# Kernel tuning notes

Hardware: AMD Instinct MI355X
Metric: run time of the kernel (lower is better)

## Reference

```python
import jax, jax.numpy as jnp
import numpy as np

TEMPERATURE = 8.0  # sqrt(d_k=64)

def setup_inputs() -> dict:
    key = jax.random.key(0)
    kq, kk, kv, km1, km2 = jax.random.split(key, 5)
    B, Lq, Lk, D = 128, 512, 512, 64
    q = jax.random.normal(kq, (B, Lq, D), dtype=jnp.float32)
    k = jax.random.normal(kk, (B, Lk, D), dtype=jnp.float32)
    v = jax.random.normal(kv, (B, Lk, D), dtype=jnp.float32)
    key_mask = jax.random.bernoulli(km1, 0.5, (B, Lq, Lk))
    query_mask = jax.random.bernoulli(km2, 0.5, (B, Lq, Lk))
    return {"q": q, "k": k, "v": v, "key_mask": key_mask, "query_mask": query_mask}

def reference(q, k, v, key_mask, query_mask):
    # attn = (q @ k^T) / temperature, pre-softmax key masking with -inf
    scores = jnp.einsum('bqd,bkd->bqk', q, k) / TEMPERATURE
    scores = jnp.where(key_mask, -jnp.inf, scores)
    attn = jax.nn.softmax(scores, axis=-1)
    # post-softmax query-row zeroing
    attn = jnp.where(query_mask, 0.0, attn)
    # dropout omitted (eval mode / deterministic reference)
    output = jnp.einsum('bqk,bkd->bqd', attn, v)
    return (output, attn)
```

## Files before the change

### kernel.cpp

```cpp
#include <hip/hip_runtime.h>
#include <hip/hip_bf16.h>

#define BATCH 128
#define LQ    512
#define LK    512
#define DH    64
#define TQ    16
#define KC    128

#define KSTR  72
#define VROW  136
#define SSTR  520

typedef float    float4v __attribute__((ext_vector_type(4)));
typedef short    short8v __attribute__((ext_vector_type(8)));
typedef short    short4v __attribute__((ext_vector_type(4)));
typedef int      int4v   __attribute__((ext_vector_type(4)));
typedef _Float16 half4v  __attribute__((ext_vector_type(4)));

__device__ __forceinline__ short bf16r(float f) {
  union { float f; unsigned u; } x; x.f = f;
  unsigned r = x.u + 0x7FFFu + ((x.u >> 16) & 1u);
  return (short)(r >> 16);
}

__global__ __launch_bounds__(256, 4)
void sdpa_kernel(const float* __restrict__ Q, const float* __restrict__ K,
                 const float* __restrict__ V, const int* __restrict__ KM,
                 const int* __restrict__ QM, float* __restrict__ OUT,
                 float* __restrict__ ATT)
{
  __shared__ short kvs[KC * KSTR];
  __shared__ short scs[TQ * SSTR];

  const int b    = blockIdx.x >> 5;
  const int q0   = (blockIdx.x & 31) * TQ;
  const int tid  = threadIdx.x;
  const int lane = tid & 63;
  const int wave = tid >> 6;
  const int lm   = lane & 15;
  const int quad = lane >> 4;

  const int row = tid >> 4;
  const int col = tid & 15;
  const size_t gro = (size_t)(b * LQ + q0 + row) * LK;

  int4v kmv[8];
#pragma unroll
  for (int j = 0; j < 8; ++j)
    kmv[j] = *(const int4v*)(KM + gro + col * 4 + j * 64);

  const float* qrow = Q + ((size_t)(b * LQ + q0 + lm)) * DH + quad * 8;
  short8v aq0, aq1;
  {
    float4v f0 = *(const float4v*)(qrow + 0);
    float4v f1 = *(const float4v*)(qrow + 4);
    float4v f2 = *(const float4v*)(qrow + 32);
    float4v f3 = *(const float4v*)(qrow + 36);
#pragma unroll
    for (int e = 0; e < 4; ++e) {
      aq0[e]     = bf16r(f0[e]);
      aq0[e + 4] = bf16r(f1[e]);
      aq1[e]     = bf16r(f2[e]);
      aq1[e + 4] = bf16r(f3[e]);
    }
  }

  for (int kt = 0; kt < LK / KC; ++kt) {
    const float* ksrc = K + ((size_t)(b * LK + kt * KC)) * DH;
#pragma unroll
    for (int i = 0; i < 8; ++i) {
      int fl = (tid + i * 256) << 2;
      int r  = fl >> 6, c = fl & 63;
      float4v d4 = *(const float4v*)(ksrc + fl);
      short4v s4;
      s4[0] = bf16r(d4[0]); s4[1] = bf16r(d4[1]);
      s4[2] = bf16r(d4[2]); s4[3] = bf16r(d4[3]);
      *(short4v*)&kvs[r * KSTR + c] = s4;
    }
    __syncthreads();
#pragma unroll
    for (int t = 0; t < 2; ++t) {
      int ntl = (wave * 2 + t) * 16;
      const short* bp = &kvs[(ntl + lm) * KSTR + quad * 8];
      short8v b0 = *(const short8v*)(bp);
      short8v b1 = *(const short8v*)(bp + 32);
      float4v acc = {0.f, 0.f, 0.f, 0.f};
      acc = __builtin_amdgcn_mfma_f32_16x16x32_bf16(aq0, b0, acc, 0, 0, 0);
      acc = __builtin_amdgcn_mfma_f32_16x16x32_bf16(aq1, b1, acc, 0, 0, 0);
      int n  = kt * KC + ntl + lm;
      int m0 = quad * 4;
#pragma unroll
      for (int j = 0; j < 4; ++j)
        *(_Float16*)&scs[(m0 + j) * SSTR + n] = (_Float16)acc[j];
    }
    __syncthreads();
  }

  float s[32];
  float mx = -INFINITY;
#pragma unroll
  for (int j = 0; j < 8; ++j) {
    half4v h4 = *(const half4v*)&scs[row * SSTR + col * 4 + j * 64];
#pragma unroll
    for (int e = 0; e < 4; ++e) {
      float val = kmv[j][e] ? -INFINITY : (float)h4[e];
      s[j * 4 + e] = val;
      mx = fmaxf(mx, val);
    }
  }
  int4v qmv[8];
#pragma unroll
  for (int j = 0; j < 8; ++j)
    qmv[j] = *(const int4v*)(QM + gro + col * 4 + j * 64);
#pragma unroll
  for (int off = 8; off; off >>= 1) mx = fmaxf(mx, __shfl_xor(mx, off, 64));
  float sum = 0.f;
#pragma unroll
  for (int j = 0; j < 32; ++j) {
    float p = __expf((s[j] - mx) * 0.125f);
    s[j] = p;
    sum += p;
  }
#pragma unroll
  for (int off = 8; off; off >>= 1) sum += __shfl_xor(sum, off, 64);
  const float inv = 1.f / sum;
  float* arow = ATT + gro;
#pragma unroll
  for (int j = 0; j < 8; ++j) {
    int kk = col * 4 + j * 64;
    float4v a4;
#pragma unroll
    for (int e = 0; e < 4; ++e)
      a4[e] = qmv[j][e] ? 0.f : s[j * 4 + e] * inv;
    *(float4v*)(arow + kk) = a4;
    short4v ab;
    ab[0] = bf16r(a4[0]); ab[1] = bf16r(a4[1]);
    ab[2] = bf16r(a4[2]); ab[3] = bf16r(a4[3]);
    *(short4v*)&scs[row * SSTR + kk] = ab;
  }

  float4v oacc = {0.f, 0.f, 0.f, 0.f};
  for (int kt = 0; kt < LK / KC; ++kt) {
    const float* vsrc = V + ((size_t)(b * LK + kt * KC)) * DH;
#pragma unroll
    for (int it = 0; it < 2; ++it) {
      int Bx = tid + 256 * it;
      int bR = Bx >> 4;
      int bC = Bx & 15;
      const float* vp = vsrc + bR * 4 * DH + bC * 4;
      float4v r0 = *(const float4v*)(vp);
      float4v r1 = *(const float4v*)(vp + DH);
      float4v r2 = *(const float4v*)(vp + 2 * DH);
      float4v r3 = *(const float4v*)(vp + 3 * DH);
#pragma unroll
      for (int e = 0; e < 4; ++e) {
        int d  = bC * 4 + e;
        int gp = bR ^ (d & 31);
        short4v s4;
        s4[0] = bf16r(r0[e]); s4[1] = bf16r(r1[e]);
        s4[2] = bf16r(r2[e]); s4[3] = bf16r(r3[e]);
        *(short4v*)&kvs[d * VROW + gp * 4] = s4;
      }
    }
    __syncthreads();
#pragma unroll
    for (int ks = 0; ks < 4; ++ks) {
      const short* ap = &scs[lm * SSTR + kt * KC + ks * 32 + quad * 8];
      short8v a8 = *(const short8v*)ap;
      int n  = wave * 16 + lm;
      int g0 = ks * 8 + quad * 2;
      short4v lo = *(const short4v*)&kvs[n * VROW + ((g0    ) ^ (n & 31)) * 4];
      short4v hi = *(const short4v*)&kvs[n * VROW + ((g0 + 1) ^ (n & 31)) * 4];
      short8v b8;
      b8[0] = lo[0]; b8[1] = lo[1]; b8[2] = lo[2]; b8[3] = lo[3];
      b8[4] = hi[0]; b8[5] = hi[1]; b8[6] = hi[2]; b8[7] = hi[3];
      oacc = __builtin_amdgcn_mfma_f32_16x16x32_bf16(a8, b8, oacc, 0, 0, 0);
    }
    __syncthreads();
  }
  {
    int m0 = quad * 4;
    float* obase = OUT + ((size_t)(b * LQ + q0 + m0)) * DH + wave * 16 + lm;
    obase[0 * DH] = oacc[0];
    obase[1 * DH] = oacc[1];
    obase[2 * DH] = oacc[2];
    obase[3 * DH] = oacc[3];
  }
}

extern "C" void kernel_launch(void* const* d_in, const int* in_sizes, int n_in,
                              void* d_out, int out_size, void* d_ws, size_t ws_size,
                              hipStream_t stream) {
  const float* q  = (const float*)d_in[0];
  const float* k  = (const float*)d_in[1];
  const float* v  = (const float*)d_in[2];
  const int*   km = (const int*)d_in[3];
  const int*   qm = (const int*)d_in[4];
  float* out  = (float*)d_out;
  float* attn = out + (size_t)BATCH * LQ * DH;
  dim3 grid(BATCH * (LQ / TQ));
  dim3 block(256);
  hipLaunchKernelGGL(sdpa_kernel, grid, block, 0, stream,
                     q, k, v, km, qm, out, attn);
}
```

Measured before the change: 378.9 us.

## Load K directly to registers, double-buffer V tiles, remap blocks, use nontemporal I/O

The QK^T phase now has each wave load its own K rows from global memory straight into MFMA operands, which removes the LDS staging and two barriers per tile. The PV phase uses 64-key tiles with register prefetch of the next V tile, overlapping the global loads with the MFMAs, and a smaller LDS footprint. Block IDs are permuted across batches and occupancy is raised to 6 blocks per SM. Mask loads and attention stores become nontemporal to avoid polluting cache. The risks are more barriers in the PV loop, higher register pressure from prefetching, and K being reread from global per wave rather than shared through LDS.

After: 404.2 us. 1.07x slower.

```diff
diff --git a/kernel.cpp b/kernel.cpp
--- a/kernel.cpp
+++ b/kernel.cpp
@@ -6,10 +6,9 @@
 #define LK    512
 #define DH    64
 #define TQ    16
-#define KC    128
-
-#define KSTR  72
-#define VROW  136
+#define KC    64
+
+#define VROW  72
 #define SSTR  520
 
 typedef float    float4v __attribute__((ext_vector_type(4)));
@@ -24,17 +23,19 @@
   return (short)(r >> 16);
 }
 
-__global__ __launch_bounds__(256, 4)
+__global__ __launch_bounds__(256, 6)
 void sdpa_kernel(const float* __restrict__ Q, const float* __restrict__ K,
                  const float* __restrict__ V, const int* __restrict__ KM,
                  const int* __restrict__ QM, float* __restrict__ OUT,
                  float* __restrict__ ATT)
 {
-  __shared__ short kvs[KC * KSTR];
+  __shared__ short kvs[KC * VROW];
   __shared__ short scs[TQ * SSTR];
 
-  const int b    = blockIdx.x >> 5;
-  const int q0   = (blockIdx.x & 31) * TQ;
+  const int bid  = blockIdx.x;
+  const int wg   = ((bid & 7) << 9) | (bid >> 3);
+  const int b    = wg >> 5;
+  const int q0   = (wg & 31) * TQ;
   const int tid  = threadIdx.x;
   const int lane = tid & 63;
   const int wave = tid >> 6;
@@ -48,7 +49,7 @@
   int4v kmv[8];
 #pragma unroll
   for (int j = 0; j < 8; ++j)
-    kmv[j] = *(const int4v*)(KM + gro + col * 4 + j * 64);
+    kmv[j] = __builtin_nontemporal_load((const int4v*)(KM + gro + col * 4 + j * 64));
 
   const float* qrow = Q + ((size_t)(b * LQ + q0 + lm)) * DH + quad * 8;
   short8v aq0, aq1;
@@ -66,36 +67,32 @@
     }
   }
 
-  for (int kt = 0; kt < LK / KC; ++kt) {
-    const float* ksrc = K + ((size_t)(b * LK + kt * KC)) * DH;
-#pragma unroll
-    for (int i = 0; i < 8; ++i) {
-      int fl = (tid + i * 256) << 2;
-      int r  = fl >> 6, c = fl & 63;
-      float4v d4 = *(const float4v*)(ksrc + fl);
-      short4v s4;
-      s4[0] = bf16r(d4[0]); s4[1] = bf16r(d4[1]);
-      s4[2] = bf16r(d4[2]); s4[3] = bf16r(d4[3]);
-      *(short4v*)&kvs[r * KSTR + c] = s4;
-    }
-    __syncthreads();
-#pragma unroll
-    for (int t = 0; t < 2; ++t) {
-      int ntl = (wave * 2 + t) * 16;
-      const short* bp = &kvs[(ntl + lm) * KSTR + quad * 8];
-      short8v b0 = *(const short8v*)(bp);
-      short8v b1 = *(const short8v*)(bp + 32);
-      float4v acc = {0.f, 0.f, 0.f, 0.f};
-      acc = __builtin_amdgcn_mfma_f32_16x16x32_bf16(aq0, b0, acc, 0, 0, 0);
-      acc = __builtin_amdgcn_mfma_f32_16x16x32_bf16(aq1, b1, acc, 0, 0, 0);
-      int n  = kt * KC + ntl + lm;
-      int m0 = quad * 4;
-#pragma unroll
-      for (int j = 0; j < 4; ++j)
-        *(_Float16*)&scs[(m0 + j) * SSTR + n] = (_Float16)acc[j];
-    }
-    __syncthreads();
-  }
+#pragma unroll
+  for (int t = 0; t < 8; ++t) {
+    const int T = wave * 8 + t;
+    const float* kr = K + ((size_t)(b * LK + T * 16 + lm)) * DH + quad * 8;
+    float4v f0 = *(const float4v*)(kr + 0);
+    float4v f1 = *(const float4v*)(kr + 4);
+    float4v f2 = *(const float4v*)(kr + 32);
+    float4v f3 = *(const float4v*)(kr + 36);
+    short8v b0, b1;
+#pragma unroll
+    for (int e = 0; e < 4; ++e) {
+      b0[e]     = bf16r(f0[e]);
+      b0[e + 4] = bf16r(f1[e]);
+      b1[e]     = bf16r(f2[e]);
+      b1[e + 4] = bf16r(f3[e]);
+    }
+    float4v acc = {0.f, 0.f, 0.f, 0.f};
+    acc = __builtin_amdgcn_mfma_f32_16x16x32_bf16(aq0, b0, acc, 0, 0, 0);
+    acc = __builtin_amdgcn_mfma_f32_16x16x32_bf16(aq1, b1, acc, 0, 0, 0);
+    const int n  = T * 16 + lm;
+    const int m0 = quad * 4;
+#pragma unroll
+    for (int j = 0; j < 4; ++j)
+      *(_Float16*)&scs[(m0 + j) * SSTR + n] = (_Float16)acc[j];
+  }
+  __syncthreads();
 
   float s[32];
   float mx = -INFINITY;
@@ -112,7 +109,7 @@
   int4v qmv[8];
 #pragma unroll
   for (int j = 0; j < 8; ++j)
-    qmv[j] = *(const int4v*)(QM + gro + col * 4 + j * 64);
+    qmv[j] = __builtin_nontemporal_load((const int4v*)(QM + gro + col * 4 + j * 64));
 #pragma unroll
   for (int off = 8; off; off >>= 1) mx = fmaxf(mx, __shfl_xor(mx, off, 64));
   float sum = 0.f;
@@ -133,7 +130,7 @@
 #pragma unroll
     for (int e = 0; e < 4; ++e)
       a4[e] = qmv[j][e] ? 0.f : s[j * 4 + e] * inv;
-    *(float4v*)(arow + kk) = a4;
+    __builtin_nontemporal_store(a4, (float4v*)(arow + kk));
     short4v ab;
     ab[0] = bf16r(a4[0]); ab[1] = bf16r(a4[1]);
     ab[2] = bf16r(a4[2]); ab[3] = bf16r(a4[3]);
@@ -141,43 +138,47 @@
   }
 
   float4v oacc = {0.f, 0.f, 0.f, 0.f};
-  for (int kt = 0; kt < LK / KC; ++kt) {
-    const float* vsrc = V + ((size_t)(b * LK + kt * KC)) * DH;
-#pragma unroll
-    for (int it = 0; it < 2; ++it) {
-      int Bx = tid + 256 * it;
-      int bR = Bx >> 4;
-      int bC = Bx & 15;
-      const float* vp = vsrc + bR * 4 * DH + bC * 4;
-      float4v r0 = *(const float4v*)(vp);
-      float4v r1 = *(const float4v*)(vp + DH);
-      float4v r2 = *(const float4v*)(vp + 2 * DH);
-      float4v r3 = *(const float4v*)(vp + 3 * DH);
-#pragma unroll
-      for (int e = 0; e < 4; ++e) {
-        int d  = bC * 4 + e;
-        int gp = bR ^ (d & 31);
-        short4v s4;
-        s4[0] = bf16r(r0[e]); s4[1] = bf16r(r1[e]);
-        s4[2] = bf16r(r2[e]); s4[3] = bf16r(r3[e]);
-        *(short4v*)&kvs[d * VROW + gp * 4] = s4;
-      }
+  const float* vbase = V + ((size_t)b * LK) * DH;
+  float4v va[4];
+  {
+    const float* vp = vbase + (row * 4) * DH + col * 4;
+#pragma unroll
+    for (int r = 0; r < 4; ++r) va[r] = *(const float4v*)(vp + r * DH);
+  }
+#pragma unroll
+  for (int kt = 0; kt < 8; ++kt) {
+#pragma unroll
+    for (int e = 0; e < 4; ++e) {
+      int d  = col * 4 + e;
+      int gp = row ^ (d & 15);
+      short4v s4;
+      s4[0] = bf16r(va[0][e]); s4[1] = bf16r(va[1][e]);
+      s4[2] = bf16r(va[2][e]); s4[3] = bf16r(va[3][e]);
+      *(short4v*)&kvs[d * VROW + gp * 4] = s4;
+    }
+    float4v vb[4];
+    if (kt < 7) {
+      const float* vp = vbase + ((kt + 1) * KC + row * 4) * DH + col * 4;
+#pragma unroll
+      for (int r = 0; r < 4; ++r) vb[r] = *(const float4v*)(vp + r * DH);
     }
     __syncthreads();
 #pragma unroll
-    for (int ks = 0; ks < 4; ++ks) {
+    for (int ks = 0; ks < 2; ++ks) {
       const short* ap = &scs[lm * SSTR + kt * KC + ks * 32 + quad * 8];
       short8v a8 = *(const short8v*)ap;
       int n  = wave * 16 + lm;
       int g0 = ks * 8 + quad * 2;
-      short4v lo = *(const short4v*)&kvs[n * VROW + ((g0    ) ^ (n & 31)) * 4];
-      short4v hi = *(const short4v*)&kvs[n * VROW + ((g0 + 1) ^ (n & 31)) * 4];
+      short4v lo = *(const short4v*)&kvs[n * VROW + ((g0    ) ^ (n & 15)) * 4];
+      short4v hi = *(const short4v*)&kvs[n * VROW + ((g0 + 1) ^ (n & 15)) * 4];
       short8v b8;
       b8[0] = lo[0]; b8[1] = lo[1]; b8[2] = lo[2]; b8[3] = lo[3];
       b8[4] = hi[0]; b8[5] = hi[1]; b8[6] = hi[2]; b8[7] = hi[3];
       oacc = __builtin_amdgcn_mfma_f32_16x16x32_bf16(a8, b8, oacc, 0, 0, 0);
     }
     __syncthreads();
+#pragma unroll
+    for (int r = 0; r < 4; ++r) va[r] = vb[r];
   }
   {
     int m0 = quad * 4;
```
